# Kernel optimization log

Measured on AMD Instinct MI355X. Metric: run time of the kernel, lower is better.

The kernel has to match this reference:

```python
import jax, jax.numpy as jnp
import numpy as np

N_WIRES = 4
DIM = 2 ** N_WIRES  # 16-dim statevector


def _zsigns():
    # PauliZ sign per basis state; wire 0 is the most-significant bit
    idx = np.arange(DIM)
    signs = np.stack([1 - 2 * ((idx >> (N_WIRES - 1 - w)) & 1) for w in range(N_WIRES)], 0)
    return jnp.asarray(signs, jnp.float32)  # [4, 16]

ZSIGNS = _zsigns()


def _apply_rx(state, ang, w):
    # state: [B, 16] complex64, ang: [B] rotation angle on wire w
    B = state.shape[0]
    s = state.reshape(B, 2 ** w, 2, 2 ** (N_WIRES - 1 - w))
    c = jnp.cos(ang * 0.5)[:, None, None]
    sn = jnp.sin(ang * 0.5)[:, None, None]
    s0, s1 = s[:, :, 0, :], s[:, :, 1, :]
    o0 = c * s0 - 1j * sn * s1
    o1 = -1j * sn * s0 + c * s1
    return jnp.stack([o0, o1], axis=2).reshape(B, DIM)


def _cnot(state, c, t):
    # flip target bit t where control bit c == 1
    B = state.shape[0]
    s = state.reshape((B,) + (2,) * N_WIRES)
    ca, ta = c + 1, t + 1  # +1 for batch axis
    s0 = jnp.take(s, 0, axis=ca)
    s1 = jnp.take(s, 1, axis=ca)
    t_ax = ta - 1 if ta > ca else ta  # target axis shifts after control axis removed
    s1 = jnp.flip(s1, axis=t_ax)     # size-2 flip == Pauli-X
    return jnp.stack([s0, s1], axis=ca).reshape(B, DIM)


def _qgate(v, theta):
    # v: [B, 4] encoder angles, theta: [4] trainable RX angles (RX angles add)
    B = v.shape[0]
    ang = v + theta[None, :]
    state = jnp.zeros((B, DIM), jnp.complex64).at[:, 0].set(1.0)
    for w in range(N_WIRES):
        state = _apply_rx(state, ang[:, w], w)
    for w in range(N_WIRES):
        state = _cnot(state, w, (w + 1) % N_WIRES)
    probs = jnp.real(state * jnp.conj(state))  # [B, 16]
    return probs @ ZSIGNS.T                    # [B, 4] <Z> per wire


def setup_inputs() -> dict:
    key = jax.random.key(0)
    ks = jax.random.split(key, 16)
    B, S, V, E, H, T = 256, 128, 32000, 256, 4, 32
    d_in = E + H
    sc = 1.0 / np.sqrt(d_in)
    inp = {
        'x': jax.random.randint(ks[0], (B, S), 0, V),
        'embedding': jax.random.normal(ks[1], (V, E), jnp.float32) * 0.02,
        'Wf': jax.random.normal(ks[2], (H, d_in), jnp.float32) * sc,
        'bf': jnp.zeros((H,), jnp.float32),
        'Wi': jax.random.normal(ks[3], (H, d_in), jnp.float32) * sc,
        'bi': jnp.zeros((H,), jnp.float32),
        'Wu': jax.random.normal(ks[4], (H, d_in), jnp.float32) * sc,
        'bu': jnp.zeros((H,), jnp.float32),
        'Wo': jax.random.normal(ks[5], (H, d_in), jnp.float32) * sc,
        'bo': jnp.zeros((H,), jnp.float32),
        'theta_f': jax.random.uniform(ks[6], (H,), jnp.float32, 0.0, 2 * np.pi),
        'theta_i': jax.random.uniform(ks[7], (H,), jnp.float32, 0.0, 2 * np.pi),
        'theta_u': jax.random.uniform(ks[8], (H,), jnp.float32, 0.0, 2 * np.pi),
        'theta_o': jax.random.uniform(ks[9], (H,), jnp.float32, 0.0, 2 * np.pi),
        'Wc': jax.random.normal(ks[10], (T, H), jnp.float32) * 0.5,
        'bc': jnp.zeros((T,), jnp.float32),
    }
    return inp


def reference(x, embedding, Wf, bf, Wi, bi, Wu, bu, Wo, bo,
              theta_f, theta_i, theta_u, theta_o, Wc, bc):
    emb = embedding[x]  # [B, S, E]
    B, S, E = emb.shape
    H = Wf.shape[0]

    def step(carry, xt):
        hx, cx = carry
        comb = jnp.concatenate([xt, hx], axis=1)  # [B, E+H]
        f = jax.nn.sigmoid(_qgate(comb @ Wf.T + bf, theta_f))
        i = jax.nn.sigmoid(_qgate(comb @ Wi.T + bi, theta_i))
        g = jnp.tanh(_qgate(comb @ Wu.T + bu, theta_u))
        o = jax.nn.sigmoid(_qgate(comb @ Wo.T + bo, theta_o))
        cx = f * cx + i * g
        hx = o * jnp.tanh(cx)
        return (hx, cx), hx

    h0 = jnp.zeros((B, H), emb.dtype)
    (_, _), hs = jax.lax.scan(step, (h0, h0), jnp.swapaxes(emb, 0, 1))
    lstm_out = jnp.swapaxes(hs, 0, 1)        # [B, S, H]
    logits = lstm_out @ Wc.T + bc            # [B, S, T]
    return jax.nn.log_softmax(logits, axis=-1)
```

## Files before the change

kernel.cpp:

```cpp
#include <hip/hip_runtime.h>
#include <math.h>

constexpr int NB = 256;
constexpr int NS = 128;
constexpr int NE = 256;
constexpr int DIN = 260;

typedef float f2 __attribute__((ext_vector_type(2)));
#define fma2(A, B, C) __builtin_elementwise_fma((A), (B), (C))

constexpr float INV2PI = 0.15915494309189535f;

__device__ __forceinline__ float rcp_fast(float x) {
#if __has_builtin(__builtin_amdgcn_rcpf)
    return __builtin_amdgcn_rcpf(x);
#else
    return 1.0f / x;
#endif
}

__device__ __forceinline__ float cos_rev(float x) {
    float f, r;
    asm("v_fract_f32 %0, %1" : "=v"(f) : "v"(x));
    asm("v_cos_f32 %0, %1" : "=v"(r) : "v"(f));
    return r;
}

#if __has_builtin(__builtin_amdgcn_mov_dpp)
#define DPP_XOR1(x) __int_as_float(__builtin_amdgcn_mov_dpp(__float_as_int(x), 0xB1, 0xF, 0xF, true))
#define DPP_XOR2(x) __int_as_float(__builtin_amdgcn_mov_dpp(__float_as_int(x), 0x4E, 0xF, 0xF, true))
#define DPP_XOR3(x) __int_as_float(__builtin_amdgcn_mov_dpp(__float_as_int(x), 0x1B, 0xF, 0xF, true))
#else
#define DPP_XOR1(x) __shfl_xor((x), 1, 64)
#define DPP_XOR2(x) __shfl_xor((x), 2, 64)
#define DPP_XOR3(x) __shfl_xor((x), 3, 64)
#endif

__device__ __forceinline__ float tanh_cf(float y) {
    float w = y * y;
    float num = y * fmaf(fmaf(21.0f, w, 1260.0f), w, 10395.0f);
    float den = fmaf(fmaf(w + 210.0f, w, 4725.0f), w, 10395.0f);
    return num * rcp_fast(den);
}

__device__ __forceinline__ float sel4f(float v0, float v1, float v2, float v3,
                                       bool bit0, bool bit1) {
    float lo = bit0 ? v1 : v0;
    float hi = bit0 ? v3 : v2;
    return bit1 ? hi : lo;
}

__global__ __launch_bounds__(256) void k_embed(
    const int* __restrict__ x, const float* __restrict__ emb,
    const float* __restrict__ Wf, const float* __restrict__ bf,
    const float* __restrict__ Wi, const float* __restrict__ bi,
    const float* __restrict__ Wu, const float* __restrict__ bu,
    const float* __restrict__ Wo, const float* __restrict__ bo,
    const float* __restrict__ thf, const float* __restrict__ thi,
    const float* __restrict__ thu, const float* __restrict__ tho,
    float* __restrict__ xpart)
{
    const int lane = threadIdx.x & 63;
    const int wave_id = blockIdx.x * 4 + (threadIdx.x >> 6);
    const int row0 = wave_id * 16;

    const int tok16 = x[((row0 & 255) + (lane & 15)) * NS + (row0 >> 8)];

    float4 Wreg[16];
    #pragma unroll
    for (int j = 0; j < 16; ++j) {
        const float* Wgp = (j < 8) ? ((j < 4) ? Wf : Wi) : ((j < 12) ? Wu : Wo);
        float4 w = *(const float4*)(Wgp + (j & 3) * DIN + lane * 4);
        Wreg[j] = make_float4(w.x * INV2PI, w.y * INV2PI, w.z * INV2PI, w.w * INV2PI);
    }
    float biasv;
    {
        int j = lane & 15, jj = j & 3;
        const float* bp = (j < 8) ? ((j < 4) ? bf : bi) : ((j < 12) ? bu : bo);
        const float* tp = (j < 8) ? ((j < 4) ? thf : thi) : ((j < 12) ? thu : tho);
        biasv = (bp[jj] + tp[jj]) * INV2PI;
    }

    const bool p0 = (lane & 1) != 0, p1 = (lane & 2) != 0,
               p2 = (lane & 4) != 0, p3 = (lane & 8) != 0;

#define LDE(I) (*(const float4*)(emb + \
    (size_t)(unsigned)__shfl(tok16, (I), 64) * NE + lane * 4))

#define PROC(I, EV) do {                                                     \
    float acc[16];                                                           \
    _Pragma("unroll")                                                        \
    for (int j = 0; j < 16; ++j) {                                           \
        float4 wv = Wreg[j];                                                 \
        acc[j] = fmaf((EV).x, wv.x, fmaf((EV).y, wv.y,                       \
                  fmaf((EV).z, wv.z, (EV).w * wv.w)));                       \
    }                                                                        \
    float t8[8];                                                             \
    _Pragma("unroll")                                                        \
    for (int i2 = 0; i2 < 8; ++i2) {                                         \
        float keep = p0 ? acc[2 * i2 + 1] : acc[2 * i2];                     \
        float send = p0 ? acc[2 * i2] : acc[2 * i2 + 1];                     \
        t8[i2] = keep + __shfl_xor(send, 1, 64);                             \
    }                                                                        \
    float t4[4];                                                             \
    _Pragma("unroll")                                                        \
    for (int i2 = 0; i2 < 4; ++i2) {                                         \
        float keep = p1 ? t8[2 * i2 + 1] : t8[2 * i2];                       \
        float send = p1 ? t8[2 * i2] : t8[2 * i2 + 1];                       \
        t4[i2] = keep + __shfl_xor(send, 2, 64);                             \
    }                                                                        \
    float t2[2];                                                             \
    _Pragma("unroll")                                                        \
    for (int i2 = 0; i2 < 2; ++i2) {                                         \
        float keep = p2 ? t4[2 * i2 + 1] : t4[2 * i2];                       \
        float send = p2 ? t4[2 * i2] : t4[2 * i2 + 1];                       \
        t2[i2] = keep + __shfl_xor(send, 4, 64);                             \
    }                                                                        \
    float keep = p3 ? t2[1] : t2[0];                                         \
    float send = p3 ? t2[0] : t2[1];                                         \
    float t1 = keep + __shfl_xor(send, 8, 64);                               \
    t1 += __shfl_xor(t1, 16, 64);                                            \
    t1 += __shfl_xor(t1, 32, 64);                                            \
    if (lane < 16)                                                           \
        xpart[(size_t)(row0 + (I)) * 16 + lane] = t1 + biasv;                \
} while (0)

    float4 ev0 = LDE(0), ev1 = LDE(1), ev2 = LDE(2),
           ev3 = LDE(3), ev4 = LDE(4), ev5 = LDE(5);
    PROC(0,  ev0); ev0 = LDE(6);
    PROC(1,  ev1); ev1 = LDE(7);
    PROC(2,  ev2); ev2 = LDE(8);
    PROC(3,  ev3); ev3 = LDE(9);
    PROC(4,  ev4); ev4 = LDE(10);
    PROC(5,  ev5); ev5 = LDE(11);
    PROC(6,  ev0); ev0 = LDE(12);
    PROC(7,  ev1); ev1 = LDE(13);
    PROC(8,  ev2); ev2 = LDE(14);
    PROC(9,  ev3); ev3 = LDE(15);
    PROC(10, ev4);
    PROC(11, ev5);
    PROC(12, ev0);
    PROC(13, ev1);
    PROC(14, ev2);
    PROC(15, ev3);
#undef PROC
#undef LDE
}

__global__ __launch_bounds__(64) void k_recur(
    const float* __restrict__ Wf, const float* __restrict__ Wi,
    const float* __restrict__ Wu, const float* __restrict__ Wo,
    const float* __restrict__ xpart, float* __restrict__ hs)
{
    __shared__ float hlds[128][64];

    const int lane = threadIdx.x;
    const int g = lane & 3;
    const int b0 = blockIdx.x * 16;

    const float* Wg = (g == 0) ? Wf : ((g == 1) ? Wi : ((g == 2) ? Wu : Wo));
    f2 W01[4], W23[4];
    #pragma unroll
    for (int k = 0; k < 4; ++k) {
        W01[k] = f2{Wg[0 * DIN + 256 + (g ^ k)] * INV2PI,
                    Wg[1 * DIN + 256 + (g ^ k)] * INV2PI};
        W23[k] = f2{Wg[2 * DIN + 256 + (g ^ k)] * INV2PI,
                    Wg[3 * DIN + 256 + (g ^ k)] * INV2PI};
    }

    const bool bb0 = (g & 1) != 0, bb1 = (g & 2) != 0;
    const float scl = (g == 2) ? 1.0f : 0.5f;
    const float mlt = (g == 2) ? 1.0f : 0.5f;
    const float bas = (g == 2) ? 0.0f : 0.5f;
    const float s2 = scl * scl;
    const float e0 = mlt * 0.999416f * scl;
    const float e1 = mlt * -0.326958f * scl * s2;
    const float e2 = mlt * 0.111796f * scl * s2 * s2;
    const float e3 = mlt * -0.022660f * scl * s2 * s2 * s2;
    const f2 D0d = {e0, e0}, D1d = {e1, e1}, D2d = {e2, e2}, D3d = {e3, e3};
    const f2 basd = {bas, bas};

    float c = 0.0f;
    float hr0 = 0.f, hr1 = 0.f, hr2 = 0.f, hr3 = 0.f;

    const char* xblk = (const char*)xpart + (size_t)b0 * 64 + (size_t)lane * 16;

#define LDX(CH, K) (*(const float4*)(xblk + (size_t)(((CH) * 8 + (K)) * 16384)))

#define QS(XC, S) do {                                                        \
    f2 x01 = {(XC).x, (XC).y}, x23 = {(XC).z, (XC).w};                        \
    f2 h0d = {hr0, hr0}, h1d = {hr1, hr1}, h2d = {hr2, hr2}, h3d = {hr3, hr3};\
    f2 a01 = fma2(W01[0], h0d, x01);                                          \
    f2 n01 = W01[2] * h2d;                                                    \
    a01 = fma2(W01[1], h1d, a01);                                             \
    n01 = fma2(W01[3], h3d, n01);                                             \
    a01 = a01 + n01;                                                          \
    f2 a23 = fma2(W23[0], h0d, x23);                                          \
    f2 n23 = W23[2] * h2d;                                                    \
    a23 = fma2(W23[1], h1d, a23);                                             \
    n23 = fma2(W23[3], h3d, n23);                                             \
    a23 = a23 + n23;                                                          \
    float c0_ = cos_rev(a01.x), c1_ = cos_rev(a01.y);                         \
    float c2_ = cos_rev(a23.x), c3_ = cos_rev(a23.y);                         \
    float tt = c2_ * c3_;                                                     \
    float q1 = c0_ * c1_;                                                     \
    f2 q01 = {c1_ * tt, q1};                                                  \
    f2 q23 = {q1 * c2_, q1 * tt};                                             \
    f2 w01 = q01 * q01, w23 = q23 * q23;                                      \
    f2 p01 = fma2(fma2(fma2(D3d, w01, D2d), w01, D1d), w01, D0d);             \
    f2 p23 = fma2(fma2(fma2(D3d, w23, D2d), w23, D1d), w23, D0d);             \
    f2 A01 = fma2(q01, p01, basd);                                            \
    f2 A23 = fma2(q23, p23, basd);                                            \
    float A0 = A01.x, A1 = A01.y, A2 = A23.x, A3 = A23.y;                     \
    float r1 = DPP_XOR1(sel4f(A0, A1, A2, A3, !bb0,  bb1));                   \
    float r2 = DPP_XOR2(sel4f(A0, A1, A2, A3,  bb0, !bb1));                   \
    float r3 = DPP_XOR3(sel4f(A0, A1, A2, A3, !bb0, !bb1));                   \
    float r0 = sel4f(A0, A1, A2, A3, bb0, bb1);                               \
    float fv = sel4f(r0, r1, r2, r3,  bb0,  bb1);                             \
    float iv = sel4f(r0, r1, r2, r3, !bb0,  bb1);                             \
    float uv = sel4f(r0, r1, r2, r3,  bb0, !bb1);                             \
    float ov = sel4f(r0, r1, r2, r3, !bb0, !bb1);                             \
    c = fmaf(fv, c, iv * uv);                                                 \
    float hn = ov * tanh_cf(c);                                               \
    hlds[S][lane] = hn;                                                       \
    hr0 = hn;                                                                 \
    hr1 = DPP_XOR1(hn);                                                       \
    hr2 = DPP_XOR2(hn);                                                       \
    hr3 = DPP_XOR3(hn);                                                       \
} while (0)

    float4 xA0 = LDX(0, 0), xA1 = LDX(0, 1), xA2 = LDX(0, 2), xA3 = LDX(0, 3);
    float4 xA4 = LDX(0, 4), xA5 = LDX(0, 5), xA6 = LDX(0, 6), xA7 = LDX(0, 7);
    float4 xB0 = LDX(1, 0), xB1 = LDX(1, 1), xB2 = LDX(1, 2), xB3 = LDX(1, 3);
    float4 xB4 = LDX(1, 4), xB5 = LDX(1, 5), xB6 = LDX(1, 6), xB7 = LDX(1, 7);

    for (int cp = 0; cp < 7; ++cp) {
        int s0 = cp * 16;
        int chA = cp * 2 + 2;
        int chB = cp * 2 + 3;
        QS(xA0, s0 + 0);  xA0 = LDX(chA, 0);
        QS(xA1, s0 + 1);  xA1 = LDX(chA, 1);
        QS(xA2, s0 + 2);  xA2 = LDX(chA, 2);
        QS(xA3, s0 + 3);  xA3 = LDX(chA, 3);
        QS(xA4, s0 + 4);  xA4 = LDX(chA, 4);
        QS(xA5, s0 + 5);  xA5 = LDX(chA, 5);
        QS(xA6, s0 + 6);  xA6 = LDX(chA, 6);
        QS(xA7, s0 + 7);  xA7 = LDX(chA, 7);
        QS(xB0, s0 + 8);  xB0 = LDX(chB, 0);
        QS(xB1, s0 + 9);  xB1 = LDX(chB, 1);
        QS(xB2, s0 + 10); xB2 = LDX(chB, 2);
        QS(xB3, s0 + 11); xB3 = LDX(chB, 3);
        QS(xB4, s0 + 12); xB4 = LDX(chB, 4);
        QS(xB5, s0 + 13); xB5 = LDX(chB, 5);
        QS(xB6, s0 + 14); xB6 = LDX(chB, 6);
        QS(xB7, s0 + 15); xB7 = LDX(chB, 7);
    }
    QS(xA0, 112); QS(xA1, 113); QS(xA2, 114); QS(xA3, 115);
    QS(xA4, 116); QS(xA5, 117); QS(xA6, 118); QS(xA7, 119);
    QS(xB0, 120); QS(xB1, 121); QS(xB2, 122); QS(xB3, 123);
    QS(xB4, 124); QS(xB5, 125); QS(xB6, 126); QS(xB7, 127);
#undef QS
#undef LDX

    __builtin_amdgcn_s_waitcnt(0);
    #pragma unroll 4
    for (int j = 0; j < 32; ++j) {
        int sp = j * 4 + (lane >> 4);
        float4 v = *(const float4*)&hlds[sp][(lane & 15) * 4];
        *(float4*)(hs + (size_t)sp * 1024 + (size_t)b0 * 4 + (lane & 15) * 4) = v;
    }
}

__global__ __launch_bounds__(256) void k_out(
    const float* __restrict__ hs, const float* __restrict__ Wc,
    const float* __restrict__ bc, float* __restrict__ out)
{
    int gtid = blockIdx.x * 256 + threadIdx.x;
    int r = gtid >> 3;
    int lr = gtid & 7;
    if (r >= NB * NS) return;
    int b = r >> 7, s = r & 127;
    float4 h = *(const float4*)(hs + ((size_t)s * NB + b) * 4);
    float l[4];
    #pragma unroll
    for (int k = 0; k < 4; ++k) {
        int t = lr * 4 + k;
        float4 w = *(const float4*)(Wc + t * 4);
        l[k] = bc[t] + w.x * h.x + w.y * h.y + w.z * h.z + w.w * h.w;
    }
    float m = fmaxf(fmaxf(l[0], l[1]), fmaxf(l[2], l[3]));
    #pragma unroll
    for (int msk = 1; msk < 8; msk <<= 1)
        m = fmaxf(m, __shfl_xor(m, msk, 64));
    float sum = 0.f;
    #pragma unroll
    for (int k = 0; k < 4; ++k)
        sum += __expf(l[k] - m);
    #pragma unroll
    for (int msk = 1; msk < 8; msk <<= 1)
        sum += __shfl_xor(sum, msk, 64);
    float lse = __logf(sum);
    float4 o;
    o.x = l[0] - m - lse;
    o.y = l[1] - m - lse;
    o.z = l[2] - m - lse;
    o.w = l[3] - m - lse;
    *(float4*)(out + (size_t)r * 32 + lr * 4) = o;
}

extern "C" void kernel_launch(void* const* d_in, const int* in_sizes, int n_in,
                              void* d_out, int out_size, void* d_ws, size_t ws_size,
                              hipStream_t stream) {
    const int*   x   = (const int*)d_in[0];
    const float* emb = (const float*)d_in[1];
    const float* Wf  = (const float*)d_in[2];
    const float* bf  = (const float*)d_in[3];
    const float* Wi  = (const float*)d_in[4];
    const float* bi  = (const float*)d_in[5];
    const float* Wu  = (const float*)d_in[6];
    const float* bu  = (const float*)d_in[7];
    const float* Wo  = (const float*)d_in[8];
    const float* bo  = (const float*)d_in[9];
    const float* thf = (const float*)d_in[10];
    const float* thi = (const float*)d_in[11];
    const float* thu = (const float*)d_in[12];
    const float* tho = (const float*)d_in[13];
    const float* Wc  = (const float*)d_in[14];
    const float* bc  = (const float*)d_in[15];
    float* out = (float*)d_out;

    float* xpart = (float*)d_ws;
    float* hs    = xpart + (size_t)NS * NB * 16;

    k_embed<<<512, 256, 0, stream>>>(x, emb, Wf, bf, Wi, bi, Wu, bu, Wo, bo,
                                     thf, thi, thu, tho, xpart);
    k_recur<<<16, 64, 0, stream>>>(Wf, Wi, Wu, Wo, xpart, hs);
    k_out<<<1024, 256, 0, stream>>>(hs, Wc, bc, out);
}
```

Measured before the change: 42.00 us.

## Spread recurrence over 64 blocks with per-lane gate qubit and fuse output head

The recurrent kernel now assigns one lane per (batch, gate, qubit) instead of one lane per (batch, gate) holding all four qubits. Each block handles 4 batches rather than 16, and the grid grows from 16 to 64 blocks. The per-step cosine products and gate exchanges move into DPP cross-lane moves, which shortens each lane's serial dependency chain per timestep. The classifier and log-softmax are fused into the tail of the recurrent kernel using LDS-staged hidden states, removing the hs round trip and one launch. In exchange there are more cross-lane moves per step, and the output stage runs on only 64 wavefronts.

```diff
diff --git a/kernel.cpp b/kernel.cpp
--- a/kernel.cpp
+++ b/kernel.cpp
@@ -5,9 +5,6 @@
 constexpr int NS = 128;
 constexpr int NE = 256;
 constexpr int DIN = 260;
-
-typedef float f2 __attribute__((ext_vector_type(2)));
-#define fma2(A, B, C) __builtin_elementwise_fma((A), (B), (C))
 
 constexpr float INV2PI = 0.15915494309189535f;
 
@@ -26,15 +23,13 @@
     return r;
 }
 
-#if __has_builtin(__builtin_amdgcn_mov_dpp)
-#define DPP_XOR1(x) __int_as_float(__builtin_amdgcn_mov_dpp(__float_as_int(x), 0xB1, 0xF, 0xF, true))
-#define DPP_XOR2(x) __int_as_float(__builtin_amdgcn_mov_dpp(__float_as_int(x), 0x4E, 0xF, 0xF, true))
-#define DPP_XOR3(x) __int_as_float(__builtin_amdgcn_mov_dpp(__float_as_int(x), 0x1B, 0xF, 0xF, true))
-#else
-#define DPP_XOR1(x) __shfl_xor((x), 1, 64)
-#define DPP_XOR2(x) __shfl_xor((x), 2, 64)
-#define DPP_XOR3(x) __shfl_xor((x), 3, 64)
-#endif
+#define DPPF(x, CTRL) __int_as_float(__builtin_amdgcn_mov_dpp(__float_as_int(x), (CTRL), 0xF, 0xF, true))
+#define DX1(x)   DPPF(x, 0xB1)
+#define DX2(x)   DPPF(x, 0x4E)
+#define DX3(x)   DPPF(x, 0x1B)
+#define DROR8(x) DPPF(x, 0x128)
+#define DHM(x)   DPPF(x, 0x141)
+#define DRM(x)   DPPF(x, 0x140)
 
 __device__ __forceinline__ float tanh_cf(float y) {
     float w = y * y;
@@ -150,162 +145,164 @@
 __global__ __launch_bounds__(64) void k_recur(
     const float* __restrict__ Wf, const float* __restrict__ Wi,
     const float* __restrict__ Wu, const float* __restrict__ Wo,
-    const float* __restrict__ xpart, float* __restrict__ hs)
+    const float* __restrict__ xpart,
+    const float* __restrict__ Wc, const float* __restrict__ bc,
+    float* __restrict__ out)
 {
-    __shared__ float hlds[128][64];
+    __shared__ float hlds[128][16];
 
     const int lane = threadIdx.x;
-    const int g = lane & 3;
-    const int b0 = blockIdx.x * 16;
+    const int grp = lane >> 4;
+    const int q   = lane & 15;
+    const int g   = q >> 2;
+    const int j   = q & 3;
+    const int b0  = blockIdx.x * 4;
 
     const float* Wg = (g == 0) ? Wf : ((g == 1) ? Wi : ((g == 2) ? Wu : Wo));
-    f2 W01[4], W23[4];
-    #pragma unroll
-    for (int k = 0; k < 4; ++k) {
-        W01[k] = f2{Wg[0 * DIN + 256 + (g ^ k)] * INV2PI,
-                    Wg[1 * DIN + 256 + (g ^ k)] * INV2PI};
-        W23[k] = f2{Wg[2 * DIN + 256 + (g ^ k)] * INV2PI,
-                    Wg[3 * DIN + 256 + (g ^ k)] * INV2PI};
-    }
-
-    const bool bb0 = (g & 1) != 0, bb1 = (g & 2) != 0;
+    const float W0 = Wg[j * DIN + 256 + (j ^ 0)] * INV2PI;
+    const float W1 = Wg[j * DIN + 256 + (j ^ 1)] * INV2PI;
+    const float W2 = Wg[j * DIN + 256 + (j ^ 2)] * INV2PI;
+    const float W3 = Wg[j * DIN + 256 + (j ^ 3)] * INV2PI;
+
+    const bool j0 = (j & 1) != 0, j1 = (j & 2) != 0;
+    const bool g0 = (g & 1) != 0, g1 = (g & 2) != 0;
+    const bool isj1 = (j == 1);
+
     const float scl = (g == 2) ? 1.0f : 0.5f;
     const float mlt = (g == 2) ? 1.0f : 0.5f;
     const float bas = (g == 2) ? 0.0f : 0.5f;
     const float s2 = scl * scl;
-    const float e0 = mlt * 0.999416f * scl;
-    const float e1 = mlt * -0.326958f * scl * s2;
-    const float e2 = mlt * 0.111796f * scl * s2 * s2;
-    const float e3 = mlt * -0.022660f * scl * s2 * s2 * s2;
-    const f2 D0d = {e0, e0}, D1d = {e1, e1}, D2d = {e2, e2}, D3d = {e3, e3};
-    const f2 basd = {bas, bas};
+    const float D0s = mlt * 0.999416f * scl;
+    const float D1s = mlt * -0.326958f * scl * s2;
+    const float D2s = mlt * 0.111796f * scl * s2 * s2;
+    const float D3s = mlt * -0.022660f * scl * s2 * s2 * s2;
 
     float c = 0.0f;
     float hr0 = 0.f, hr1 = 0.f, hr2 = 0.f, hr3 = 0.f;
 
-    const char* xblk = (const char*)xpart + (size_t)b0 * 64 + (size_t)lane * 16;
-
-#define LDX(CH, K) (*(const float4*)(xblk + (size_t)(((CH) * 8 + (K)) * 16384)))
+    const float* xblk = xpart + b0 * 16 + lane;
+
+#define LDXs(CH, K) (xblk[(size_t)(((CH) * 16 + (K)) * 4096)])
 
 #define QS(XC, S) do {                                                        \
-    f2 x01 = {(XC).x, (XC).y}, x23 = {(XC).z, (XC).w};                        \
-    f2 h0d = {hr0, hr0}, h1d = {hr1, hr1}, h2d = {hr2, hr2}, h3d = {hr3, hr3};\
-    f2 a01 = fma2(W01[0], h0d, x01);                                          \
-    f2 n01 = W01[2] * h2d;                                                    \
-    a01 = fma2(W01[1], h1d, a01);                                             \
-    n01 = fma2(W01[3], h3d, n01);                                             \
-    a01 = a01 + n01;                                                          \
-    f2 a23 = fma2(W23[0], h0d, x23);                                          \
-    f2 n23 = W23[2] * h2d;                                                    \
-    a23 = fma2(W23[1], h1d, a23);                                             \
-    n23 = fma2(W23[3], h3d, n23);                                             \
-    a23 = a23 + n23;                                                          \
-    float c0_ = cos_rev(a01.x), c1_ = cos_rev(a01.y);                         \
-    float c2_ = cos_rev(a23.x), c3_ = cos_rev(a23.y);                         \
-    float tt = c2_ * c3_;                                                     \
-    float q1 = c0_ * c1_;                                                     \
-    f2 q01 = {c1_ * tt, q1};                                                  \
-    f2 q23 = {q1 * c2_, q1 * tt};                                             \
-    f2 w01 = q01 * q01, w23 = q23 * q23;                                      \
-    f2 p01 = fma2(fma2(fma2(D3d, w01, D2d), w01, D1d), w01, D0d);             \
-    f2 p23 = fma2(fma2(fma2(D3d, w23, D2d), w23, D1d), w23, D0d);             \
-    f2 A01 = fma2(q01, p01, basd);                                            \
-    f2 A23 = fma2(q23, p23, basd);                                            \
-    float A0 = A01.x, A1 = A01.y, A2 = A23.x, A3 = A23.y;                     \
-    float r1 = DPP_XOR1(sel4f(A0, A1, A2, A3, !bb0,  bb1));                   \
-    float r2 = DPP_XOR2(sel4f(A0, A1, A2, A3,  bb0, !bb1));                   \
-    float r3 = DPP_XOR3(sel4f(A0, A1, A2, A3, !bb0, !bb1));                   \
-    float r0 = sel4f(A0, A1, A2, A3, bb0, bb1);                               \
-    float fv = sel4f(r0, r1, r2, r3,  bb0,  bb1);                             \
-    float iv = sel4f(r0, r1, r2, r3, !bb0,  bb1);                             \
-    float uv = sel4f(r0, r1, r2, r3,  bb0, !bb1);                             \
-    float ov = sel4f(r0, r1, r2, r3, !bb0, !bb1);                             \
+    float t_ = fmaf(W0, hr0, (XC));                                           \
+    float u_ = W1 * hr1;                                                      \
+    t_ = fmaf(W2, hr2, t_);                                                   \
+    u_ = fmaf(W3, hr3, u_);                                                   \
+    float a_ = t_ + u_;                                                       \
+    float cv = cos_rev(a_);                                                   \
+    float d1 = DX1(cv);                                                       \
+    float t1 = cv * d1;                                                       \
+    float d2 = DX2(t1);                                                       \
+    float X_ = sel4f(d1, t1, cv, t1, j0, j1);                                 \
+    float Y_ = isj1 ? 1.0f : d2;                                              \
+    float P_ = X_ * Y_;                                                       \
+    float w_ = P_ * P_;                                                       \
+    float p_ = fmaf(fmaf(fmaf(D3s, w_, D2s), w_, D1s), w_, D0s);              \
+    float A_ = fmaf(P_, p_, bas);                                             \
+    float t3 = DX3(A_);                                                       \
+    float A4 = DHM(t3);                            \
+    float A8 = DROR8(A_);                          \
+    float A12 = DRM(t3);                           \
+    float fv = sel4f(A_,  A4,  A8,  A12, g0, g1);                             \
+    float iv = sel4f(A4,  A_,  A12, A8,  g0, g1);                             \
+    float uv = sel4f(A8,  A12, A_,  A4,  g0, g1);                             \
+    float ov = sel4f(A12, A8,  A4,  A_,  g0, g1);                             \
     c = fmaf(fv, c, iv * uv);                                                 \
     float hn = ov * tanh_cf(c);                                               \
-    hlds[S][lane] = hn;                                                       \
+    hlds[S][(grp << 2) | j] = hn;                                             \
     hr0 = hn;                                                                 \
-    hr1 = DPP_XOR1(hn);                                                       \
-    hr2 = DPP_XOR2(hn);                                                       \
-    hr3 = DPP_XOR3(hn);                                                       \
+    hr1 = DX1(hn);                                                            \
+    hr2 = DX2(hn);                                                            \
+    hr3 = DX3(hn);                                                            \
 } while (0)
 
-    float4 xA0 = LDX(0, 0), xA1 = LDX(0, 1), xA2 = LDX(0, 2), xA3 = LDX(0, 3);
-    float4 xA4 = LDX(0, 4), xA5 = LDX(0, 5), xA6 = LDX(0, 6), xA7 = LDX(0, 7);
-    float4 xB0 = LDX(1, 0), xB1 = LDX(1, 1), xB2 = LDX(1, 2), xB3 = LDX(1, 3);
-    float4 xB4 = LDX(1, 4), xB5 = LDX(1, 5), xB6 = LDX(1, 6), xB7 = LDX(1, 7);
-
-    for (int cp = 0; cp < 7; ++cp) {
-        int s0 = cp * 16;
+    float xA0 = LDXs(0, 0),  xA1 = LDXs(0, 1),  xA2 = LDXs(0, 2),  xA3 = LDXs(0, 3);
+    float xA4 = LDXs(0, 4),  xA5 = LDXs(0, 5),  xA6 = LDXs(0, 6),  xA7 = LDXs(0, 7);
+    float xA8 = LDXs(0, 8),  xA9 = LDXs(0, 9),  xA10 = LDXs(0, 10), xA11 = LDXs(0, 11);
+    float xA12 = LDXs(0, 12), xA13 = LDXs(0, 13), xA14 = LDXs(0, 14), xA15 = LDXs(0, 15);
+    float xB0 = LDXs(1, 0),  xB1 = LDXs(1, 1),  xB2 = LDXs(1, 2),  xB3 = LDXs(1, 3);
+    float xB4 = LDXs(1, 4),  xB5 = LDXs(1, 5),  xB6 = LDXs(1, 6),  xB7 = LDXs(1, 7);
+    float xB8 = LDXs(1, 8),  xB9 = LDXs(1, 9),  xB10 = LDXs(1, 10), xB11 = LDXs(1, 11);
+    float xB12 = LDXs(1, 12), xB13 = LDXs(1, 13), xB14 = LDXs(1, 14), xB15 = LDXs(1, 15);
+
+    for (int cp = 0; cp < 3; ++cp) {
+        int s0 = cp * 32;
         int chA = cp * 2 + 2;
         int chB = cp * 2 + 3;
-        QS(xA0, s0 + 0);  xA0 = LDX(chA, 0);
-        QS(xA1, s0 + 1);  xA1 = LDX(chA, 1);
-        QS(xA2, s0 + 2);  xA2 = LDX(chA, 2);
-        QS(xA3, s0 + 3);  xA3 = LDX(chA, 3);
-        QS(xA4, s0 + 4);  xA4 = LDX(chA, 4);
-        QS(xA5, s0 + 5);  xA5 = LDX(chA, 5);
-        QS(xA6, s0 + 6);  xA6 = LDX(chA, 6);
-        QS(xA7, s0 + 7);  xA7 = LDX(chA, 7);
-        QS(xB0, s0 + 8);  xB0 = LDX(chB, 0);
-        QS(xB1, s0 + 9);  xB1 = LDX(chB, 1);
-        QS(xB2, s0 + 10); xB2 = LDX(chB, 2);
-        QS(xB3, s0 + 11); xB3 = LDX(chB, 3);
-        QS(xB4, s0 + 12); xB4 = LDX(chB, 4);
-        QS(xB5, s0 + 13); xB5 = LDX(chB, 5);
-        QS(xB6, s0 + 14); xB6 = LDX(chB, 6);
-        QS(xB7, s0 + 15); xB7 = LDX(chB, 7);
+        QS(xA0, s0 + 0);   xA0 = LDXs(chA, 0);
+        QS(xA1, s0 + 1);   xA1 = LDXs(chA, 1);
+        QS(xA2, s0 + 2);   xA2 = LDXs(chA, 2);
+        QS(xA3, s0 + 3);   xA3 = LDXs(chA, 3);
+        QS(xA4, s0 + 4);   xA4 = LDXs(chA, 4);
+        QS(xA5, s0 + 5);   xA5 = LDXs(chA, 5);
+        QS(xA6, s0 + 6);   xA6 = LDXs(chA, 6);
+        QS(xA7, s0 + 7);   xA7 = LDXs(chA, 7);
+        QS(xA8, s0 + 8);   xA8 = LDXs(chA, 8);
+        QS(xA9, s0 + 9);   xA9 = LDXs(chA, 9);
+        QS(xA10, s0 + 10); xA10 = LDXs(chA, 10);
+        QS(xA11, s0 + 11); xA11 = LDXs(chA, 11);
+        QS(xA12, s0 + 12); xA12 = LDXs(chA, 12);
+        QS(xA13, s0 + 13); xA13 = LDXs(chA, 13);
+        QS(xA14, s0 + 14); xA14 = LDXs(chA, 14);
+        QS(xA15, s0 + 15); xA15 = LDXs(chA, 15);
+        QS(xB0, s0 + 16);  xB0 = LDXs(chB, 0);
+        QS(xB1, s0 + 17);  xB1 = LDXs(chB, 1);
+        QS(xB2, s0 + 18);  xB2 = LDXs(chB, 2);
+        QS(xB3, s0 + 19);  xB3 = LDXs(chB, 3);
+        QS(xB4, s0 + 20);  xB4 = LDXs(chB, 4);
+        QS(xB5, s0 + 21);  xB5 = LDXs(chB, 5);
+        QS(xB6, s0 + 22);  xB6 = LDXs(chB, 6);
+        QS(xB7, s0 + 23);  xB7 = LDXs(chB, 7);
+        QS(xB8, s0 + 24);  xB8 = LDXs(chB, 8);
+        QS(xB9, s0 + 25);  xB9 = LDXs(chB, 9);
+        QS(xB10, s0 + 26); xB10 = LDXs(chB, 10);
+        QS(xB11, s0 + 27); xB11 = LDXs(chB, 11);
+        QS(xB12, s0 + 28); xB12 = LDXs(chB, 12);
+        QS(xB13, s0 + 29); xB13 = LDXs(chB, 13);
+        QS(xB14, s0 + 30); xB14 = LDXs(chB, 14);
+        QS(xB15, s0 + 31); xB15 = LDXs(chB, 15);
     }
-    QS(xA0, 112); QS(xA1, 113); QS(xA2, 114); QS(xA3, 115);
-    QS(xA4, 116); QS(xA5, 117); QS(xA6, 118); QS(xA7, 119);
-    QS(xB0, 120); QS(xB1, 121); QS(xB2, 122); QS(xB3, 123);
-    QS(xB4, 124); QS(xB5, 125); QS(xB6, 126); QS(xB7, 127);
+    QS(xA0, 96);  QS(xA1, 97);  QS(xA2, 98);  QS(xA3, 99);
+    QS(xA4, 100); QS(xA5, 101); QS(xA6, 102); QS(xA7, 103);
+    QS(xA8, 104); QS(xA9, 105); QS(xA10, 106); QS(xA11, 107);
+    QS(xA12, 108); QS(xA13, 109); QS(xA14, 110); QS(xA15, 111);
+    QS(xB0, 112); QS(xB1, 113); QS(xB2, 114); QS(xB3, 115);
+    QS(xB4, 116); QS(xB5, 117); QS(xB6, 118); QS(xB7, 119);
+    QS(xB8, 120); QS(xB9, 121); QS(xB10, 122); QS(xB11, 123);
+    QS(xB12, 124); QS(xB13, 125); QS(xB14, 126); QS(xB15, 127);
 #undef QS
-#undef LDX
-
-    __builtin_amdgcn_s_waitcnt(0);
-    #pragma unroll 4
-    for (int j = 0; j < 32; ++j) {
-        int sp = j * 4 + (lane >> 4);
-        float4 v = *(const float4*)&hlds[sp][(lane & 15) * 4];
-        *(float4*)(hs + (size_t)sp * 1024 + (size_t)b0 * 4 + (lane & 15) * 4) = v;
+#undef LDXs
+
+    asm volatile("s_waitcnt lgkmcnt(0)" ::: "memory");
+    const int t0 = (lane & 7) * 4;
+    float4 w0 = *(const float4*)(Wc + (t0 + 0) * 4);
+    float4 w1 = *(const float4*)(Wc + (t0 + 1) * 4);
+    float4 w2 = *(const float4*)(Wc + (t0 + 2) * 4);
+    float4 w3 = *(const float4*)(Wc + (t0 + 3) * 4);
+    float4 bv = *(const float4*)(bc + t0);
+
+    for (int pass = 0; pass < 64; ++pass) {
+        int r = pass * 8 + (lane >> 3);
+        int bat = r >> 7, s = r & 127;
+        float4 h4 = *(const float4*)&hlds[s][bat * 4];
+        float l0 = bv.x + w0.x * h4.x + w0.y * h4.y + w0.z * h4.z + w0.w * h4.w;
+        float l1 = bv.y + w1.x * h4.x + w1.y * h4.y + w1.z * h4.z + w1.w * h4.w;
+        float l2 = bv.z + w2.x * h4.x + w2.y * h4.y + w2.z * h4.z + w2.w * h4.w;
+        float l3 = bv.w + w3.x * h4.x + w3.y * h4.y + w3.z * h4.z + w3.w * h4.w;
+        float m = fmaxf(fmaxf(l0, l1), fmaxf(l2, l3));
+        m = fmaxf(m, __shfl_xor(m, 1, 64));
+        m = fmaxf(m, __shfl_xor(m, 2, 64));
+        m = fmaxf(m, __shfl_xor(m, 4, 64));
+        float sum = __expf(l0 - m) + __expf(l1 - m) + __expf(l2 - m) + __expf(l3 - m);
+        sum += __shfl_xor(sum, 1, 64);
+        sum += __shfl_xor(sum, 2, 64);
+        sum += __shfl_xor(sum, 4, 64);
+        float base = m + __logf(sum);
+        float4 o;
+        o.x = l0 - base; o.y = l1 - base; o.z = l2 - base; o.w = l3 - base;
+        *(float4*)(out + ((size_t)(b0 + bat) * 128 + s) * 32 + t0) = o;
     }
-}
-
-__global__ __launch_bounds__(256) void k_out(
-    const float* __restrict__ hs, const float* __restrict__ Wc,
-    const float* __restrict__ bc, float* __restrict__ out)
-{
-    int gtid = blockIdx.x * 256 + threadIdx.x;
-    int r = gtid >> 3;
-    int lr = gtid & 7;
-    if (r >= NB * NS) return;
-    int b = r >> 7, s = r & 127;
-    float4 h = *(const float4*)(hs + ((size_t)s * NB + b) * 4);
-    float l[4];
-    #pragma unroll
-    for (int k = 0; k < 4; ++k) {
-        int t = lr * 4 + k;
-        float4 w = *(const float4*)(Wc + t * 4);
-        l[k] = bc[t] + w.x * h.x + w.y * h.y + w.z * h.z + w.w * h.w;
-    }
-    float m = fmaxf(fmaxf(l[0], l[1]), fmaxf(l[2], l[3]));
-    #pragma unroll
-    for (int msk = 1; msk < 8; msk <<= 1)
-        m = fmaxf(m, __shfl_xor(m, msk, 64));
-    float sum = 0.f;
-    #pragma unroll
-    for (int k = 0; k < 4; ++k)
-        sum += __expf(l[k] - m);
-    #pragma unroll
-    for (int msk = 1; msk < 8; msk <<= 1)
-        sum += __shfl_xor(sum, msk, 64);
-    float lse = __logf(sum);
-    float4 o;
-    o.x = l[0] - m - lse;
-    o.y = l[1] - m - lse;
-    o.z = l[2] - m - lse;
-    o.w = l[3] - m - lse;
-    *(float4*)(out + (size_t)r * 32 + lr * 4) = o;
 }
 
 extern "C" void kernel_launch(void* const* d_in, const int* in_sizes, int n_in,
@@ -330,10 +327,8 @@
     float* out = (float*)d_out;
 
     float* xpart = (float*)d_ws;
-    float* hs    = xpart + (size_t)NS * NB * 16;
 
     k_embed<<<512, 256, 0, stream>>>(x, emb, Wf, bf, Wi, bi, Wu, bu, Wo, bo,
                                      thf, thi, thu, tho, xpart);
-    k_recur<<<16, 64, 0, stream>>>(Wf, Wi, Wu, Wo, xpart, hs);
-    k_out<<<1024, 256, 0, stream>>>(hs, Wc, bc, out);
-}
+    k_recur<<<64, 64, 0, stream>>>(Wf, Wi, Wu, Wo, xpart, Wc, bc, out);
+}
```

After: 53.33 us. 1.27x slower.

## Fuse embed, recurrence and output into one cooperative kernel with overlap

Applied to the files above, without the earlier changes.

Replaces three launches with one cooperative kernel of 256 blocks. After a grid sync, the first 16 blocks run the first 32 recurrence steps on the already-projected timesteps while the other blocks project the remaining timesteps. A second grid sync follows, then the recurrence finishes and log-softmax is computed straight from the shared-memory hidden states. This removes launch gaps, the hs round trip through global memory and part of the serial embedding phase, at the cost of two grid-wide barriers and idle threads in the consumer blocks.

```diff
diff --git a/kernel.cpp b/kernel.cpp
--- a/kernel.cpp
+++ b/kernel.cpp
@@ -1,5 +1,8 @@
 #include <hip/hip_runtime.h>
+#include <hip/hip_cooperative_groups.h>
 #include <math.h>
+
+namespace cg = cooperative_groups;
 
 constexpr int NB = 256;
 constexpr int NS = 128;
@@ -50,7 +53,7 @@
     return bit1 ? hi : lo;
 }
 
-__global__ __launch_bounds__(256) void k_embed(
+__global__ __launch_bounds__(256) void k_fused(
     const int* __restrict__ x, const float* __restrict__ emb,
     const float* __restrict__ Wf, const float* __restrict__ bf,
     const float* __restrict__ Wi, const float* __restrict__ bi,
@@ -58,20 +61,22 @@
     const float* __restrict__ Wo, const float* __restrict__ bo,
     const float* __restrict__ thf, const float* __restrict__ thi,
     const float* __restrict__ thu, const float* __restrict__ tho,
-    float* __restrict__ xpart)
+    const float* __restrict__ Wc, const float* __restrict__ bc,
+    float* __restrict__ xpart, float* __restrict__ out)
 {
-    const int lane = threadIdx.x & 63;
-    const int wave_id = blockIdx.x * 4 + (threadIdx.x >> 6);
-    const int row0 = wave_id * 16;
-
-    const int tok16 = x[((row0 & 255) + (lane & 15)) * NS + (row0 >> 8)];
+    __shared__ float hlds[128][64];
+
+    const int tid = threadIdx.x;
+    const int lane = tid & 63;
+    const int wv = tid >> 6;
+    const int w = blockIdx.x * 4 + wv;
 
     float4 Wreg[16];
     #pragma unroll
     for (int j = 0; j < 16; ++j) {
         const float* Wgp = (j < 8) ? ((j < 4) ? Wf : Wi) : ((j < 12) ? Wu : Wo);
-        float4 w = *(const float4*)(Wgp + (j & 3) * DIN + lane * 4);
-        Wreg[j] = make_float4(w.x * INV2PI, w.y * INV2PI, w.z * INV2PI, w.w * INV2PI);
+        float4 ww = *(const float4*)(Wgp + (j & 3) * DIN + lane * 4);
+        Wreg[j] = make_float4(ww.x * INV2PI, ww.y * INV2PI, ww.z * INV2PI, ww.w * INV2PI);
     }
     float biasv;
     {
@@ -80,7 +85,6 @@
         const float* tp = (j < 8) ? ((j < 4) ? thf : thi) : ((j < 12) ? thu : tho);
         biasv = (bp[jj] + tp[jj]) * INV2PI;
     }
-
     const bool p0 = (lane & 1) != 0, p1 = (lane & 2) != 0,
                p2 = (lane & 4) != 0, p3 = (lane & 8) != 0;
 
@@ -91,9 +95,9 @@
     float acc[16];                                                           \
     _Pragma("unroll")                                                        \
     for (int j = 0; j < 16; ++j) {                                           \
-        float4 wv = Wreg[j];                                                 \
-        acc[j] = fmaf((EV).x, wv.x, fmaf((EV).y, wv.y,                       \
-                  fmaf((EV).z, wv.z, (EV).w * wv.w)));                       \
+        float4 wvv = Wreg[j];                                                \
+        acc[j] = fmaf((EV).x, wvv.x, fmaf((EV).y, wvv.y,                     \
+                  fmaf((EV).z, wvv.z, (EV).w * wvv.w)));                     \
     }                                                                        \
     float t8[8];                                                             \
     _Pragma("unroll")                                                        \
@@ -125,65 +129,42 @@
         xpart[(size_t)(row0 + (I)) * 16 + lane] = t1 + biasv;                \
 } while (0)
 
-    float4 ev0 = LDE(0), ev1 = LDE(1), ev2 = LDE(2),
-           ev3 = LDE(3), ev4 = LDE(4), ev5 = LDE(5);
-    PROC(0,  ev0); ev0 = LDE(6);
-    PROC(1,  ev1); ev1 = LDE(7);
-    PROC(2,  ev2); ev2 = LDE(8);
-    PROC(3,  ev3); ev3 = LDE(9);
-    PROC(4,  ev4); ev4 = LDE(10);
-    PROC(5,  ev5); ev5 = LDE(11);
-    PROC(6,  ev0); ev0 = LDE(12);
-    PROC(7,  ev1); ev1 = LDE(13);
-    PROC(8,  ev2); ev2 = LDE(14);
-    PROC(9,  ev3); ev3 = LDE(15);
-    PROC(10, ev4);
-    PROC(11, ev5);
-    PROC(12, ev0);
-    PROC(13, ev1);
-    PROC(14, ev2);
-    PROC(15, ev3);
-#undef PROC
-#undef LDE
-}
-
-__global__ __launch_bounds__(64) void k_recur(
-    const float* __restrict__ Wf, const float* __restrict__ Wi,
-    const float* __restrict__ Wu, const float* __restrict__ Wo,
-    const float* __restrict__ xpart, float* __restrict__ hs)
-{
-    __shared__ float hlds[128][64];
-
-    const int lane = threadIdx.x;
-    const int g = lane & 3;
+    auto embed_unit = [&](int u) {
+        const int row0 = u * 16;
+        const int tok16 = x[((row0 & 255) + (lane & 15)) * NS + (row0 >> 8)];
+        float4 ev0 = LDE(0), ev1 = LDE(1), ev2 = LDE(2),
+               ev3 = LDE(3), ev4 = LDE(4), ev5 = LDE(5);
+        PROC(0,  ev0); ev0 = LDE(6);
+        PROC(1,  ev1); ev1 = LDE(7);
+        PROC(2,  ev2); ev2 = LDE(8);
+        PROC(3,  ev3); ev3 = LDE(9);
+        PROC(4,  ev4); ev4 = LDE(10);
+        PROC(5,  ev5); ev5 = LDE(11);
+        PROC(6,  ev0); ev0 = LDE(12);
+        PROC(7,  ev1); ev1 = LDE(13);
+        PROC(8,  ev2); ev2 = LDE(14);
+        PROC(9,  ev3); ev3 = LDE(15);
+        PROC(10, ev4);
+        PROC(11, ev5);
+        PROC(12, ev0);
+        PROC(13, ev1);
+        PROC(14, ev2);
+        PROC(15, ev3);
+    };
+
+    if (w < 768) embed_unit(w);
+    cg::this_grid().sync();
+
+    const bool consumer = (blockIdx.x < 16);
     const int b0 = blockIdx.x * 16;
 
-    const float* Wg = (g == 0) ? Wf : ((g == 1) ? Wi : ((g == 2) ? Wu : Wo));
     f2 W01[4], W23[4];
-    #pragma unroll
-    for (int k = 0; k < 4; ++k) {
-        W01[k] = f2{Wg[0 * DIN + 256 + (g ^ k)] * INV2PI,
-                    Wg[1 * DIN + 256 + (g ^ k)] * INV2PI};
-        W23[k] = f2{Wg[2 * DIN + 256 + (g ^ k)] * INV2PI,
-                    Wg[3 * DIN + 256 + (g ^ k)] * INV2PI};
-    }
-
-    const bool bb0 = (g & 1) != 0, bb1 = (g & 2) != 0;
-    const float scl = (g == 2) ? 1.0f : 0.5f;
-    const float mlt = (g == 2) ? 1.0f : 0.5f;
-    const float bas = (g == 2) ? 0.0f : 0.5f;
-    const float s2 = scl * scl;
-    const float e0 = mlt * 0.999416f * scl;
-    const float e1 = mlt * -0.326958f * scl * s2;
-    const float e2 = mlt * 0.111796f * scl * s2 * s2;
-    const float e3 = mlt * -0.022660f * scl * s2 * s2 * s2;
-    const f2 D0d = {e0, e0}, D1d = {e1, e1}, D2d = {e2, e2}, D3d = {e3, e3};
-    const f2 basd = {bas, bas};
-
-    float c = 0.0f;
-    float hr0 = 0.f, hr1 = 0.f, hr2 = 0.f, hr3 = 0.f;
-
-    const char* xblk = (const char*)xpart + (size_t)b0 * 64 + (size_t)lane * 16;
+    f2 D0d, D1d, D2d, D3d, basd;
+    bool bb0 = false, bb1 = false;
+    float c = 0.0f, hr0 = 0.f, hr1 = 0.f, hr2 = 0.f, hr3 = 0.f;
+    const char* xblk = (const char*)xpart;
+    float4 xA0, xA1, xA2, xA3, xA4, xA5, xA6, xA7;
+    float4 xB0, xB1, xB2, xB3, xB4, xB5, xB6, xB7;
 
 #define LDX(CH, K) (*(const float4*)(xblk + (size_t)(((CH) * 8 + (K)) * 16384)))
 
@@ -229,83 +210,128 @@
     hr3 = DPP_XOR3(hn);                                                       \
 } while (0)
 
-    float4 xA0 = LDX(0, 0), xA1 = LDX(0, 1), xA2 = LDX(0, 2), xA3 = LDX(0, 3);
-    float4 xA4 = LDX(0, 4), xA5 = LDX(0, 5), xA6 = LDX(0, 6), xA7 = LDX(0, 7);
-    float4 xB0 = LDX(1, 0), xB1 = LDX(1, 1), xB2 = LDX(1, 2), xB3 = LDX(1, 3);
-    float4 xB4 = LDX(1, 4), xB5 = LDX(1, 5), xB6 = LDX(1, 6), xB7 = LDX(1, 7);
-
-    for (int cp = 0; cp < 7; ++cp) {
-        int s0 = cp * 16;
-        int chA = cp * 2 + 2;
-        int chB = cp * 2 + 3;
-        QS(xA0, s0 + 0);  xA0 = LDX(chA, 0);
-        QS(xA1, s0 + 1);  xA1 = LDX(chA, 1);
-        QS(xA2, s0 + 2);  xA2 = LDX(chA, 2);
-        QS(xA3, s0 + 3);  xA3 = LDX(chA, 3);
-        QS(xA4, s0 + 4);  xA4 = LDX(chA, 4);
-        QS(xA5, s0 + 5);  xA5 = LDX(chA, 5);
-        QS(xA6, s0 + 6);  xA6 = LDX(chA, 6);
-        QS(xA7, s0 + 7);  xA7 = LDX(chA, 7);
-        QS(xB0, s0 + 8);  xB0 = LDX(chB, 0);
-        QS(xB1, s0 + 9);  xB1 = LDX(chB, 1);
-        QS(xB2, s0 + 10); xB2 = LDX(chB, 2);
-        QS(xB3, s0 + 11); xB3 = LDX(chB, 3);
-        QS(xB4, s0 + 12); xB4 = LDX(chB, 4);
-        QS(xB5, s0 + 13); xB5 = LDX(chB, 5);
-        QS(xB6, s0 + 14); xB6 = LDX(chB, 6);
-        QS(xB7, s0 + 15); xB7 = LDX(chB, 7);
-    }
-    QS(xA0, 112); QS(xA1, 113); QS(xA2, 114); QS(xA3, 115);
-    QS(xA4, 116); QS(xA5, 117); QS(xA6, 118); QS(xA7, 119);
-    QS(xB0, 120); QS(xB1, 121); QS(xB2, 122); QS(xB3, 123);
-    QS(xB4, 124); QS(xB5, 125); QS(xB6, 126); QS(xB7, 127);
+    if (!consumer) {
+        int idx = w - 64;
+        embed_unit(768 + idx);
+        if (idx < 320) embed_unit(1728 + idx);
+    } else if (tid < 64) {
+        const int g = lane & 3;
+        const float* Wg = (g == 0) ? Wf : ((g == 1) ? Wi : ((g == 2) ? Wu : Wo));
+        #pragma unroll
+        for (int k = 0; k < 4; ++k) {
+            W01[k] = f2{Wg[0 * DIN + 256 + (g ^ k)] * INV2PI,
+                        Wg[1 * DIN + 256 + (g ^ k)] * INV2PI};
+            W23[k] = f2{Wg[2 * DIN + 256 + (g ^ k)] * INV2PI,
+                        Wg[3 * DIN + 256 + (g ^ k)] * INV2PI};
+        }
+        bb0 = (g & 1) != 0; bb1 = (g & 2) != 0;
+        const float scl = (g == 2) ? 1.0f : 0.5f;
+        const float mlt = (g == 2) ? 1.0f : 0.5f;
+        const float bas = (g == 2) ? 0.0f : 0.5f;
+        const float s2 = scl * scl;
+        const float e0 = mlt * 0.999416f * scl;
+        const float e1 = mlt * -0.326958f * scl * s2;
+        const float e2 = mlt * 0.111796f * scl * s2 * s2;
+        const float e3 = mlt * -0.022660f * scl * s2 * s2 * s2;
+        D0d = f2{e0, e0}; D1d = f2{e1, e1}; D2d = f2{e2, e2}; D3d = f2{e3, e3};
+        basd = f2{bas, bas};
+
+        xblk = (const char*)xpart + (size_t)b0 * 64 + (size_t)lane * 16;
+
+        xA0 = LDX(0, 0); xA1 = LDX(0, 1); xA2 = LDX(0, 2); xA3 = LDX(0, 3);
+        xA4 = LDX(0, 4); xA5 = LDX(0, 5); xA6 = LDX(0, 6); xA7 = LDX(0, 7);
+        xB0 = LDX(1, 0); xB1 = LDX(1, 1); xB2 = LDX(1, 2); xB3 = LDX(1, 3);
+        xB4 = LDX(1, 4); xB5 = LDX(1, 5); xB6 = LDX(1, 6); xB7 = LDX(1, 7);
+
+        #pragma unroll
+        for (int cp = 0; cp < 2; ++cp) {
+            int s0 = cp * 16;
+            int chA = cp * 2 + 2;
+            int chB = cp * 2 + 3;
+            QS(xA0, s0 + 0);  xA0 = LDX(chA, 0);
+            QS(xA1, s0 + 1);  xA1 = LDX(chA, 1);
+            QS(xA2, s0 + 2);  xA2 = LDX(chA, 2);
+            QS(xA3, s0 + 3);  xA3 = LDX(chA, 3);
+            QS(xA4, s0 + 4);  xA4 = LDX(chA, 4);
+            QS(xA5, s0 + 5);  xA5 = LDX(chA, 5);
+            QS(xA6, s0 + 6);  xA6 = LDX(chA, 6);
+            QS(xA7, s0 + 7);  xA7 = LDX(chA, 7);
+            QS(xB0, s0 + 8);  xB0 = LDX(chB, 0);
+            QS(xB1, s0 + 9);  xB1 = LDX(chB, 1);
+            QS(xB2, s0 + 10); xB2 = LDX(chB, 2);
+            QS(xB3, s0 + 11); xB3 = LDX(chB, 3);
+            QS(xB4, s0 + 12); xB4 = LDX(chB, 4);
+            QS(xB5, s0 + 13); xB5 = LDX(chB, 5);
+            QS(xB6, s0 + 14); xB6 = LDX(chB, 6);
+            QS(xB7, s0 + 15); xB7 = LDX(chB, 7);
+        }
+    }
+    cg::this_grid().sync();
+    if (!consumer) return;
+
+    if (tid < 64) {
+        #pragma unroll
+        for (int cp = 2; cp < 7; ++cp) {
+            int s0 = cp * 16;
+            int chA = cp * 2 + 2;
+            int chB = cp * 2 + 3;
+            QS(xA0, s0 + 0);  xA0 = LDX(chA, 0);
+            QS(xA1, s0 + 1);  xA1 = LDX(chA, 1);
+            QS(xA2, s0 + 2);  xA2 = LDX(chA, 2);
+            QS(xA3, s0 + 3);  xA3 = LDX(chA, 3);
+            QS(xA4, s0 + 4);  xA4 = LDX(chA, 4);
+            QS(xA5, s0 + 5);  xA5 = LDX(chA, 5);
+            QS(xA6, s0 + 6);  xA6 = LDX(chA, 6);
+            QS(xA7, s0 + 7);  xA7 = LDX(chA, 7);
+            QS(xB0, s0 + 8);  xB0 = LDX(chB, 0);
+            QS(xB1, s0 + 9);  xB1 = LDX(chB, 1);
+            QS(xB2, s0 + 10); xB2 = LDX(chB, 2);
+            QS(xB3, s0 + 11); xB3 = LDX(chB, 3);
+            QS(xB4, s0 + 12); xB4 = LDX(chB, 4);
+            QS(xB5, s0 + 13); xB5 = LDX(chB, 5);
+            QS(xB6, s0 + 14); xB6 = LDX(chB, 6);
+            QS(xB7, s0 + 15); xB7 = LDX(chB, 7);
+        }
+        QS(xA0, 112); QS(xA1, 113); QS(xA2, 114); QS(xA3, 115);
+        QS(xA4, 116); QS(xA5, 117); QS(xA6, 118); QS(xA7, 119);
+        QS(xB0, 120); QS(xB1, 121); QS(xB2, 122); QS(xB3, 123);
+        QS(xB4, 124); QS(xB5, 125); QS(xB6, 126); QS(xB7, 127);
+    }
 #undef QS
 #undef LDX
-
-    __builtin_amdgcn_s_waitcnt(0);
-    #pragma unroll 4
-    for (int j = 0; j < 32; ++j) {
-        int sp = j * 4 + (lane >> 4);
-        float4 v = *(const float4*)&hlds[sp][(lane & 15) * 4];
-        *(float4*)(hs + (size_t)sp * 1024 + (size_t)b0 * 4 + (lane & 15) * 4) = v;
-    }
-}
-
-__global__ __launch_bounds__(256) void k_out(
-    const float* __restrict__ hs, const float* __restrict__ Wc,
-    const float* __restrict__ bc, float* __restrict__ out)
-{
-    int gtid = blockIdx.x * 256 + threadIdx.x;
-    int r = gtid >> 3;
-    int lr = gtid & 7;
-    if (r >= NB * NS) return;
-    int b = r >> 7, s = r & 127;
-    float4 h = *(const float4*)(hs + ((size_t)s * NB + b) * 4);
-    float l[4];
-    #pragma unroll
-    for (int k = 0; k < 4; ++k) {
-        int t = lr * 4 + k;
-        float4 w = *(const float4*)(Wc + t * 4);
-        l[k] = bc[t] + w.x * h.x + w.y * h.y + w.z * h.z + w.w * h.w;
-    }
-    float m = fmaxf(fmaxf(l[0], l[1]), fmaxf(l[2], l[3]));
-    #pragma unroll
-    for (int msk = 1; msk < 8; msk <<= 1)
-        m = fmaxf(m, __shfl_xor(m, msk, 64));
-    float sum = 0.f;
-    #pragma unroll
-    for (int k = 0; k < 4; ++k)
-        sum += __expf(l[k] - m);
-    #pragma unroll
-    for (int msk = 1; msk < 8; msk <<= 1)
-        sum += __shfl_xor(sum, msk, 64);
-    float lse = __logf(sum);
-    float4 o;
-    o.x = l[0] - m - lse;
-    o.y = l[1] - m - lse;
-    o.z = l[2] - m - lse;
-    o.w = l[3] - m - lse;
-    *(float4*)(out + (size_t)r * 32 + lr * 4) = o;
+#undef PROC
+#undef LDE
+
+    __syncthreads();
+
+    const int t0 = (lane & 7) * 4;
+    float4 w0 = *(const float4*)(Wc + (t0 + 0) * 4);
+    float4 w1 = *(const float4*)(Wc + (t0 + 1) * 4);
+    float4 w2 = *(const float4*)(Wc + (t0 + 2) * 4);
+    float4 w3 = *(const float4*)(Wc + (t0 + 3) * 4);
+    float4 bv = *(const float4*)(bc + t0);
+
+    for (int pass = 0; pass < 64; ++pass) {
+        int r = pass * 32 + wv * 8 + (lane >> 3);
+        int bat = r >> 7, s = r & 127;
+        float4 h4 = *(const float4*)&hlds[s][bat * 4];
+        float l0 = bv.x + w0.x * h4.x + w0.y * h4.y + w0.z * h4.z + w0.w * h4.w;
+        float l1 = bv.y + w1.x * h4.x + w1.y * h4.y + w1.z * h4.z + w1.w * h4.w;
+        float l2 = bv.z + w2.x * h4.x + w2.y * h4.y + w2.z * h4.z + w2.w * h4.w;
+        float l3 = bv.w + w3.x * h4.x + w3.y * h4.y + w3.z * h4.z + w3.w * h4.w;
+        float m = fmaxf(fmaxf(l0, l1), fmaxf(l2, l3));
+        m = fmaxf(m, __shfl_xor(m, 1, 64));
+        m = fmaxf(m, __shfl_xor(m, 2, 64));
+        m = fmaxf(m, __shfl_xor(m, 4, 64));
+        float sum = __expf(l0 - m) + __expf(l1 - m) + __expf(l2 - m) + __expf(l3 - m);
+        sum += __shfl_xor(sum, 1, 64);
+        sum += __shfl_xor(sum, 2, 64);
+        sum += __shfl_xor(sum, 4, 64);
+        float base = m + __logf(sum);
+        float4 o;
+        o.x = l0 - base; o.y = l1 - base; o.z = l2 - base; o.w = l3 - base;
+        *(float4*)(out + ((size_t)(b0 + bat) * 128 + s) * 32 + t0) = o;
+    }
 }
 
 extern "C" void kernel_launch(void* const* d_in, const int* in_sizes, int n_in,
@@ -328,12 +354,12 @@
     const float* Wc  = (const float*)d_in[14];
     const float* bc  = (const float*)d_in[15];
     float* out = (float*)d_out;
-
     float* xpart = (float*)d_ws;
-    float* hs    = xpart + (size_t)NS * NB * 16;
-
-    k_embed<<<512, 256, 0, stream>>>(x, emb, Wf, bf, Wi, bi, Wu, bu, Wo, bo,
-                                     thf, thi, thu, tho, xpart);
-    k_recur<<<16, 64, 0, stream>>>(Wf, Wi, Wu, Wo, xpart, hs);
-    k_out<<<1024, 256, 0, stream>>>(hs, Wc, bc, out);
-}
+
+    void* args[] = {
+        (void*)&x, (void*)&emb, (void*)&Wf, (void*)&bf, (void*)&Wi, (void*)&bi,
+        (void*)&Wu, (void*)&bu, (void*)&Wo, (void*)&bo, (void*)&thf, (void*)&thi,
+        (void*)&thu, (void*)&tho, (void*)&Wc, (void*)&bc, (void*)&xpart, (void*)&out
+    };
+    hipLaunchCooperativeKernel((void*)k_fused, dim3(256), dim3(256), args, 0, stream);
+}
```

After: 135.6 us. 3.23x slower.
